# Kernel tuning notes

Hardware: AMD Instinct MI355X
Metric: run time of the kernel (lower is better)

Reference implementation:

```python
import jax, jax.numpy as jnp
import numpy as np

WS = 8          # window_size
SHIFT = 4       # shift_size
HEADS = 12
C = 384
HD = C // HEADS
SCALE = HD ** -0.5
N = WS * WS


def _rel_pos_index(Wh, Ww):
    # double_step_seq(2*Ww-1, Wh, 1, Ww) -> (1, Wh*Ww); idx = rel + rel.T; flip along axis 1
    seq1 = np.arange(0, (2 * Ww - 1) * Wh, 2 * Ww - 1)
    seq2 = np.arange(0, Ww)
    rel = (seq1[:, None] + seq2[None, :]).reshape(1, -1)
    idx = rel + rel.T
    return np.flip(idx, 1).copy()

REL_IDX = jnp.asarray(_rel_pos_index(WS, WS))  # [N, N] int


def window_partition(x, ws):
    # x: [B, H, W, C] -> [B*nW, ws*ws, C]
    B, H, W, Cc = x.shape
    x = x.reshape(B, H // ws, ws, W // ws, ws, Cc).transpose(0, 1, 3, 2, 4, 5)
    return x.reshape(-1, ws * ws, Cc)


def window_reverse(win, H, W, ws):
    B = win.shape[0] // ((H // ws) * (W // ws))
    x = win.reshape(B, H // ws, W // ws, ws, ws, -1).transpose(0, 1, 3, 2, 4, 5)
    return x.reshape(B, H, W, -1)


def _attn_mask(H, W, ws, shift):
    # region ids 0..8 per (h,w) as in the torch slice loop
    hi = np.arange(H)
    wi = np.arange(W)
    h_id = (hi >= H - ws).astype(np.int32) + (hi >= H - shift).astype(np.int32)
    w_id = (wi >= W - ws).astype(np.int32) + (wi >= W - shift).astype(np.int32)
    cnt = (h_id[:, None] * 3 + w_id[None, :]).astype(np.float32)
    img = jnp.asarray(cnt)[None, :, :, None]              # [1, H, W, 1]
    mw = window_partition(img, ws).reshape(-1, ws * ws)   # [nW, N]
    diff = mw[:, None, :] - mw[:, :, None]                # [nW, N, N]
    return jnp.where(diff != 0, jnp.float32(-100.0), jnp.float32(0.0))


def setup_inputs() -> dict:
    key = jax.random.key(0)
    ks = jax.random.split(key, 8)
    B, H, W = 16, 96, 96
    std = 0.02
    return {
        "query": jax.random.normal(ks[0], (B, H * W, C), jnp.float32),
        "skip_query": jax.random.normal(ks[1], (B, H * W, C), jnp.float32),
        "W_qkv": jax.random.normal(ks[2], (C, 2 * C), jnp.float32) * std,
        "b_qkv": jnp.zeros((2 * C,), jnp.float32),
        "W_skip": jax.random.normal(ks[3], (C, C), jnp.float32) * std,
        "b_skip": jnp.zeros((C,), jnp.float32),
        "rpb_table": jax.random.normal(ks[4], ((2 * WS - 1) * (2 * WS - 1), HEADS), jnp.float32) * std,
        "W_proj": jax.random.normal(ks[5], (C, C), jnp.float32) * std,
        "b_proj": jnp.zeros((C,), jnp.float32),
        "h": H,
        "w": W,
    }


def reference(query, skip_query, W_qkv, b_qkv, W_skip, b_skip, rpb_table, W_proj, b_proj, h, w):
    B, L, Cc = query.shape
    q4 = query.reshape(B, h, w, Cc)
    s4 = skip_query.reshape(B, h, w, Cc)
    pad_r = (WS - w % WS) % WS
    pad_b = (WS - h % WS) % WS
    q4 = jnp.pad(q4, ((0, 0), (0, pad_b), (0, pad_r), (0, 0)))
    s4 = jnp.pad(s4, ((0, 0), (0, pad_b), (0, pad_r), (0, 0)))
    H_pad, W_pad = q4.shape[1], q4.shape[2]

    # cyclic shift
    q4 = jnp.roll(q4, (-SHIFT, -SHIFT), axis=(1, 2))
    s4 = jnp.roll(s4, (-SHIFT, -SHIFT), axis=(1, 2))
    mask = _attn_mask(H_pad, W_pad, WS, SHIFT)  # [nW, N, N]

    xw = window_partition(q4, WS)   # [Bn, N, C] -> k, v source
    sw = window_partition(s4, WS)   # [Bn, N, C] -> q source
    Bn = xw.shape[0]

    kv = (xw @ W_qkv + b_qkv).reshape(Bn, N, 2, HEADS, HD)
    k = kv[:, :, 0].transpose(0, 2, 1, 3)   # [Bn, H, N, d]
    v = kv[:, :, 1].transpose(0, 2, 1, 3)
    q = ((sw @ W_skip + b_skip).reshape(Bn, N, HEADS, HD).transpose(0, 2, 1, 3)) * SCALE

    attn = jnp.einsum('bhnd,bhmd->bhnm', q, k)  # [Bn, H, N, N]
    rpb = rpb_table[REL_IDX.reshape(-1)].reshape(N, N, HEADS).transpose(2, 0, 1)
    attn = attn + rpb[None]
    nW = mask.shape[0]
    attn = (attn.reshape(B, nW, HEADS, N, N) + mask[None, :, None]).reshape(Bn, HEADS, N, N)
    attn = jax.nn.softmax(attn, axis=-1)

    out = jnp.einsum('bhnm,bhmd->bhnd', attn, v).transpose(0, 2, 1, 3).reshape(Bn, N, Cc)
    out = out @ W_proj + b_proj

    x4 = window_reverse(out.reshape(-1, WS, WS, Cc), H_pad, W_pad, WS)
    x4 = jnp.roll(x4, (SHIFT, SHIFT), axis=(1, 2))
    x4 = x4[:, :h, :w]
    return x4.reshape(B, h * w, Cc)
```

## Files before the change

### kernel.cpp

```cpp
#include <hip/hip_runtime.h>
#include <hip/hip_bf16.h>


typedef __attribute__((ext_vector_type(8))) short short8;
typedef __attribute__((ext_vector_type(4))) float floatx4;

#define MFMA16(a, b, c) __builtin_amdgcn_mfma_f32_16x16x32_bf16(a, b, c, 0, 0, 0)

__device__ __forceinline__ short f2bf(float f) {
    __hip_bfloat16 h = __float2bfloat16(f);
    return *reinterpret_cast<short*>(&h);
}

__device__ __forceinline__ unsigned cvt2bf(float lo, float hi) {
    unsigned r;
    asm("v_cvt_pk_bf16_f32 %0, %1, %2" : "=v"(r) : "v"(lo), "v"(hi));
    return r;
}

__device__ __forceinline__ void glds16(const void* g, void* l) {
    __builtin_amdgcn_global_load_lds(
        (const __attribute__((address_space(1))) void*)g,
        (__attribute__((address_space(3))) void*)l, 16, 0, 0);
}


__global__ __launch_bounds__(256) void prep_wt(const float* __restrict__ Wqkv,
                                               const float* __restrict__ Wskip,
                                               short* __restrict__ Wt) {
    int tid = blockIdx.x * 256 + threadIdx.x;
    if (tid >= 384 * 144) return;
    int k = tid / 144;
    int n8 = (tid % 144) * 8;
#pragma unroll
    for (int e = 0; e < 8; e++) {
        int n = n8 + e;
        float v = (n < 768) ? Wqkv[k * 768 + n]
                            : Wskip[k * 384 + (n - 768)] * 0.17677669529663687f;
        Wt[(size_t)n * 384 + k] = f2bf(v);
    }
}

__global__ __launch_bounds__(256) void prep_wtp(const float* __restrict__ Wproj,
                                                short* __restrict__ WtP) {
    int tid = blockIdx.x * 256 + threadIdx.x;
    if (tid >= 384 * 48) return;
    int k = tid / 48;
    int n8 = (tid % 48) * 8;
#pragma unroll
    for (int e = 0; e < 8; e++) {
        int n = n8 + e;
        WtP[(size_t)n * 384 + k] = f2bf(Wproj[k * 384 + n]);
    }
}

__global__ __launch_bounds__(256) void prep_bias(const float* __restrict__ rpb,
                                                 float* __restrict__ bias64) {
    int tid = blockIdx.x * 256 + threadIdx.x;
    if (tid >= 49152) return;
    int h = tid >> 12;
    int rem = tid & 4095;
    int i = rem >> 6, kk = rem & 63;
    int j = 63 - kk;
    int ridx = 15 * (i >> 3) + (i & 7) + 15 * (j >> 3) + (j & 7);
    bias64[tid] = rpb[ridx * 12 + h];
}

__global__ __launch_bounds__(256) void gemm_qkv(
    const float* __restrict__ xq, const float* __restrict__ xs,
    const short* __restrict__ Wt,
    const float* __restrict__ bqkv, const float* __restrict__ bskip,
    short* __restrict__ kbuf, short* __restrict__ vtbuf, short* __restrict__ qbuf) {
    __shared__ short smem[36864];
    const int ABASE = 24576;

    const int win = blockIdx.x;
    const int var = blockIdx.y;
    const int nb0 = var ? 6 : 0;
    const int nbN = var ? 3 : 6;
    const float* __restrict__ src = var ? xs : xq;

    const int tid = threadIdx.x, lane = tid & 63, wid = tid >> 6;
    const int l15 = lane & 15, g4 = lane >> 4;
    const int wm = wid >> 1, wn = wid & 1;

    {
        int r = tid >> 2, q4 = tid & 3;
        int b = win / 144, wr = win % 144;
        int wy = wr / 12, wx = wr % 12;
        int yy = wy * 8 + (r >> 3) + 4; if (yy >= 96) yy -= 96;
        int xx = wx * 8 + (r & 7) + 4;  if (xx >= 96) xx -= 96;
        const float* rbase = src + ((size_t)b * 9216 + yy * 96 + xx) * 384;
        short* lrow = smem + r * 384;
        int r7 = r & 7;
#pragma unroll
        for (int j = 0; j < 12; j++) {
            int c = q4 + j * 4;
            float4 f0 = *(const float4*)(rbase + c * 8);
            float4 f1 = *(const float4*)(rbase + c * 8 + 4);
            uint4 u;
            u.x = cvt2bf(f0.x, f0.y); u.y = cvt2bf(f0.z, f0.w);
            u.z = cvt2bf(f1.x, f1.y); u.w = cvt2bf(f1.z, f1.w);
            *(uint4*)(lrow + ((c ^ r7) * 8)) = u;
        }
    }

    int browoff[2], bdst[2];
#pragma unroll
    for (int j = 0; j < 2; j++) {
        int c0 = wid * 128 + j * 64;
        int c = c0 + lane;
        int brow = c >> 2, bs = c & 3;
        int sw = (brow ^ (brow >> 2)) & 3;
        browoff[j] = brow * 384 + (bs ^ sw) * 8;
        bdst[j] = ABASE + c0 * 8;
    }

    int arow[2];
#pragma unroll
    for (int b = 0; b < 2; b++) arow[b] = (wm * 32 + b * 16 + l15) * 384;
    const int al7 = l15 & 7;
    const int xsw = (g4 ^ ((l15 ^ (l15 >> 2)) & 3)) * 8;
    int brof[4];
#pragma unroll
    for (int nj = 0; nj < 4; nj++) brof[nj] = ABASE + (wn * 64 + nj * 16 + l15) * 32 + xsw;

    {
        const short* p0 = Wt + (size_t)nb0 * 49152;
#pragma unroll
        for (int j = 0; j < 2; j++) glds16(p0 + browoff[j], smem + bdst[j]);
#pragma unroll
        for (int j = 0; j < 2; j++) glds16(p0 + browoff[j] + 32, smem + bdst[j] + 4096);
    }
    __syncthreads();

    const short* bp = Wt + (size_t)nb0 * 49152;
    for (int pb = 0; pb < nbN; ++pb) {
        const int nb = nb0 + pb;
        const bool isv = (nb >= 3 && nb < 6);
        const bool lastp = (pb == nbN - 1);
        floatx4 acc[4][2];
        floatx4 accv[2][4];
#pragma unroll
        for (int a = 0; a < 4; a++)
#pragma unroll
            for (int b = 0; b < 2; b++)
#pragma unroll
                for (int r = 0; r < 4; r++) { acc[a][b][r] = 0.f; }
#pragma unroll
        for (int a = 0; a < 2; a++)
#pragma unroll
            for (int b = 0; b < 4; b++)
#pragma unroll
                for (int r = 0; r < 4; r++) { accv[a][b][r] = 0.f; }

#pragma unroll
        for (int kt = 0; kt < 12; ++kt) {
            const int hR = kt % 3;
            const int choff = ((kt * 4 + g4) ^ al7) * 8;
            short8 af[2], bfr[4];
#pragma unroll
            for (int b = 0; b < 2; b++)
                af[b] = *(const short8*)(smem + arow[b] + choff);
#pragma unroll
            for (int nj = 0; nj < 4; nj++)
                bfr[nj] = *(const short8*)(smem + brof[nj] + hR * 4096);
            if (!lastp || kt < 10) {
                const short* ps = (kt < 10) ? bp : (bp + 49152);
                const int ko = (kt < 10) ? (kt + 2) * 32 : (kt - 10) * 32;
                const int hW = (kt + 2) % 3;
#pragma unroll
                for (int j = 0; j < 2; j++)
                    glds16(ps + browoff[j] + ko, smem + bdst[j] + hW * 4096);
            }
            if (isv) {
#pragma unroll
                for (int a = 0; a < 2; a++)
#pragma unroll
                    for (int b = 0; b < 4; b++)
                        accv[a][b] = MFMA16(af[a], bfr[b], accv[a][b]);
            } else {
#pragma unroll
                for (int a = 0; a < 4; a++)
#pragma unroll
                    for (int b = 0; b < 2; b++)
                        acc[a][b] = MFMA16(bfr[a], af[b], acc[a][b]);
            }
            if (lastp && kt == 10) {
                asm volatile("s_waitcnt vmcnt(0)" ::: "memory");
            } else {
                asm volatile("s_waitcnt vmcnt(2)" ::: "memory");
            }
            __builtin_amdgcn_s_barrier();
        }

        const int ncol0 = nb * 128 + wn * 64;
        if (!isv) {
            short* buf;
            const float* bias;
            float scl;
            if (nb < 3) { buf = kbuf; bias = bqkv; scl = 1.0f; }
            else        { buf = qbuf; bias = bskip; scl = 0.17677669529663687f; }
#pragma unroll
            for (int a = 0; a < 4; a++) {
                int nbase = ncol0 + a * 16 + g4 * 4;
                int nm = (nb < 3) ? nbase : (nbase - 768);
                int head = nm >> 5, d0 = nm & 31;
                float4 bv = *(const float4*)(bias + nm);
                short* dst = buf + (size_t)(win * 12 + head) * 2048 + d0;
#pragma unroll
                for (int b = 0; b < 2; b++) {
                    int t = wm * 32 + b * 16 + l15;
                    uint2 pk;
                    pk.x = cvt2bf(acc[a][b][0] + bv.x * scl, acc[a][b][1] + bv.y * scl);
                    pk.y = cvt2bf(acc[a][b][2] + bv.z * scl, acc[a][b][3] + bv.w * scl);
                    *(uint2*)(dst + (size_t)t * 32) = pk;
                }
            }
        } else {
#pragma unroll
            for (int nj = 0; nj < 4; nj++) {
                int nm = ncol0 + nj * 16 + l15 - 384;
                int head = nm >> 5, d = nm & 31;
                float bvs = bqkv[384 + nm];
                short* dst = vtbuf + ((size_t)(win * 12 + head) * 32 + d) * 64;
#pragma unroll
                for (int mi = 0; mi < 2; mi++) {
                    int t0 = wm * 32 + mi * 16 + g4 * 4;
                    uint2 pk;
                    pk.x = cvt2bf(accv[mi][nj][0] + bvs, accv[mi][nj][1] + bvs);
                    pk.y = cvt2bf(accv[mi][nj][2] + bvs, accv[mi][nj][3] + bvs);
                    *(uint2*)(dst + t0) = pk;
                }
            }
        }
        bp += 49152;
    }
}

__global__ __launch_bounds__(256) void attn_kernel(
    const short* __restrict__ kbuf, const short* __restrict__ vtbuf,
    const short* __restrict__ qbuf, const float* __restrict__ bias64,
    short* __restrict__ aout, int ntask) {
    __shared__ short lps[18432];
    int lane = threadIdx.x & 63, wid = threadIdx.x >> 6;
    int task = blockIdx.x * 4 + wid;
    if (task >= ntask) return;
    int win = task / 12, head = task % 12;
    int l15 = lane & 15, g4 = lane >> 4;

    const short* kb = kbuf + (size_t)task * 2048;
    const short* qb = qbuf + (size_t)task * 2048;
    const short* vb = vtbuf + (size_t)task * 2048;

    short8 kf[4], qf[4], vf[2][2];
#pragma unroll
    for (int mi = 0; mi < 4; mi++)
        kf[mi] = *(const short8*)(kb + (mi * 16 + l15) * 32 + g4 * 8);
#pragma unroll
    for (int nj = 0; nj < 4; nj++)
        qf[nj] = *(const short8*)(qb + (nj * 16 + l15) * 32 + g4 * 8);
#pragma unroll
    for (int ma = 0; ma < 2; ma++)
#pragma unroll
        for (int ks = 0; ks < 2; ks++)
            vf[ma][ks] = *(const short8*)(vb + (ma * 16 + l15) * 64 + ks * 32 + g4 * 8);

    floatx4 st[4][4];
#pragma unroll
    for (int mi = 0; mi < 4; mi++)
#pragma unroll
        for (int nj = 0; nj < 4; nj++)
#pragma unroll
            for (int r = 0; r < 4; r++) st[mi][nj][r] = 0.f;

#pragma unroll
    for (int mi = 0; mi < 4; mi++)
#pragma unroll
        for (int nj = 0; nj < 4; nj++)
            st[mi][nj] = MFMA16(kf[mi], qf[nj], st[mi][nj]);

    const float* bb = bias64 + head * 4096;
#pragma unroll
    for (int nj = 0; nj < 4; nj++) {
        int i = nj * 16 + l15;
#pragma unroll
        for (int mi = 0; mi < 4; mi++) {
            floatx4 b4 = *(const floatx4*)(bb + i * 64 + mi * 16 + g4 * 4);
            st[mi][nj] += b4;
        }
    }

    int wr = win % 144;
    int wy = wr / 12, wx = wr % 12;
    if (wy == 11 || wx == 11) {
        int wy11 = (wy == 11), wx11 = (wx == 11);
        int ri[4];
#pragma unroll
        for (int nj = 0; nj < 4; nj++) {
            int t = nj * 16 + l15;
            int hh = wy11 ? (((t >> 3) >= 4) ? 2 : 1) : 0;
            int ww = wx11 ? (((t & 7) >= 4) ? 2 : 1) : 0;
            ri[nj] = hh * 3 + ww;
        }
#pragma unroll
        for (int mi = 0; mi < 4; mi++)
#pragma unroll
            for (int r = 0; r < 4; r++) {
                int t = mi * 16 + g4 * 4 + r;
                int hh = wy11 ? (((t >> 3) >= 4) ? 2 : 1) : 0;
                int ww = wx11 ? (((t & 7) >= 4) ? 2 : 1) : 0;
                int rk = hh * 3 + ww;
#pragma unroll
                for (int nj = 0; nj < 4; nj++)
                    if (rk != ri[nj]) st[mi][nj][r] -= 100.0f;
            }
    }

    float rden[4];
#pragma unroll
    for (int nj = 0; nj < 4; nj++) {
        float m = -1e30f;
#pragma unroll
        for (int mi = 0; mi < 4; mi++)
#pragma unroll
            for (int r = 0; r < 4; r++) m = fmaxf(m, st[mi][nj][r]);
        m = fmaxf(m, __shfl_xor(m, 16));
        m = fmaxf(m, __shfl_xor(m, 32));
        float s = 0.f;
#pragma unroll
        for (int mi = 0; mi < 4; mi++)
#pragma unroll
            for (int r = 0; r < 4; r++) {
                float p = __expf(st[mi][nj][r] - m);
                st[mi][nj][r] = p;
                s += p;
            }
        s += __shfl_xor(s, 16);
        s += __shfl_xor(s, 32);
        rden[nj] = 1.0f / s;
    }

    short* Lp = lps + wid * 4608;
#pragma unroll
    for (int mi = 0; mi < 4; mi++)
#pragma unroll
        for (int nj = 0; nj < 4; nj++) {
            uint2 pk;
            pk.x = cvt2bf(st[mi][nj][0], st[mi][nj][1]);
            pk.y = cvt2bf(st[mi][nj][2], st[mi][nj][3]);
            *(uint2*)(Lp + (nj * 16 + l15) * 72 + mi * 16 + g4 * 4) = pk;
        }

    floatx4 o[2][4];
#pragma unroll
    for (int ma = 0; ma < 2; ma++)
#pragma unroll
        for (int nj = 0; nj < 4; nj++)
#pragma unroll
            for (int r = 0; r < 4; r++) o[ma][nj][r] = 0.f;
#pragma unroll
    for (int ks = 0; ks < 2; ks++) {
        short8 pb[4];
#pragma unroll
        for (int nj = 0; nj < 4; nj++)
            pb[nj] = *(const short8*)(Lp + (nj * 16 + l15) * 72 + ks * 32 + g4 * 8);
#pragma unroll
        for (int ma = 0; ma < 2; ma++)
#pragma unroll
            for (int nj = 0; nj < 4; nj++)
                o[ma][nj] = MFMA16(vf[ma][ks], pb[nj], o[ma][nj]);
    }

    short* ob = aout + (size_t)win * 64 * 384 + head * 32;
#pragma unroll
    for (int ma = 0; ma < 2; ma++)
#pragma unroll
        for (int nj = 0; nj < 4; nj++) {
            int i = nj * 16 + l15;
            uint2 pk;
            pk.x = cvt2bf(o[ma][nj][0] * rden[nj], o[ma][nj][1] * rden[nj]);
            pk.y = cvt2bf(o[ma][nj][2] * rden[nj], o[ma][nj][3] * rden[nj]);
            *(uint2*)(ob + (size_t)i * 384 + ma * 16 + g4 * 4) = pk;
        }
}

__global__ __launch_bounds__(256) void gemm_proj(
    const short* __restrict__ aout, const short* __restrict__ WtP,
    const float* __restrict__ bproj, float* __restrict__ out) {
    __shared__ short smem[36864];
    const int ABASE = 24576;

    const int win = blockIdx.x;
    const int m0 = win * 64;
    const int tid = threadIdx.x, lane = tid & 63, wid = tid >> 6;
    const int l15 = lane & 15, g4 = lane >> 4;
    const int wm = wid >> 1, wn = wid & 1;

#pragma unroll
    for (int j = 0; j < 12; j++) {
        int i = wid * 12 + j;
        int c = i * 64 + lane;
        int row = c / 48, ch = c - row * 48;
        const short* s = aout + (size_t)(m0 + row) * 384 + ((ch ^ (row & 7)) * 8);
        glds16(s, smem + i * 512);
    }

    int browoff[2], bdst[2];
#pragma unroll
    for (int j = 0; j < 2; j++) {
        int c0 = wid * 128 + j * 64;
        int c = c0 + lane;
        int brow = c >> 2, bs = c & 3;
        int sw = (brow ^ (brow >> 2)) & 3;
        browoff[j] = brow * 384 + (bs ^ sw) * 8;
        bdst[j] = ABASE + c0 * 8;
    }

    int arow[2];
#pragma unroll
    for (int b = 0; b < 2; b++) arow[b] = (wm * 32 + b * 16 + l15) * 384;
    const int al7 = l15 & 7;
    const int xsw = (g4 ^ ((l15 ^ (l15 >> 2)) & 3)) * 8;
    int brof[4];
#pragma unroll
    for (int nj = 0; nj < 4; nj++) brof[nj] = ABASE + (wn * 64 + nj * 16 + l15) * 32 + xsw;

    {
#pragma unroll
        for (int j = 0; j < 2; j++) glds16(WtP + browoff[j], smem + bdst[j]);
#pragma unroll
        for (int j = 0; j < 2; j++) glds16(WtP + browoff[j] + 32, smem + bdst[j] + 4096);
    }
    __syncthreads();

    const int b_img = win / 144, wrw = win % 144;
    const int wy = wrw / 12, wx = wrw % 12;

    const short* bp = WtP;
    for (int pb = 0; pb < 3; ++pb) {
        const bool lastp = (pb == 2);
        floatx4 acc[4][2];
#pragma unroll
        for (int a = 0; a < 4; a++)
#pragma unroll
            for (int b = 0; b < 2; b++)
#pragma unroll
                for (int r = 0; r < 4; r++) acc[a][b][r] = 0.f;

#pragma unroll
        for (int kt = 0; kt < 12; ++kt) {
            const int hR = kt % 3;
            const int choff = ((kt * 4 + g4) ^ al7) * 8;
            short8 af[2], bfr[4];
#pragma unroll
            for (int b = 0; b < 2; b++)
                af[b] = *(const short8*)(smem + arow[b] + choff);
#pragma unroll
            for (int nj = 0; nj < 4; nj++)
                bfr[nj] = *(const short8*)(smem + brof[nj] + hR * 4096);
            if (!lastp || kt < 10) {
                const short* ps = (kt < 10) ? bp : (bp + 49152);
                const int ko = (kt < 10) ? (kt + 2) * 32 : (kt - 10) * 32;
                const int hW = (kt + 2) % 3;
#pragma unroll
                for (int j = 0; j < 2; j++)
                    glds16(ps + browoff[j] + ko, smem + bdst[j] + hW * 4096);
            }
#pragma unroll
            for (int a = 0; a < 4; a++)
#pragma unroll
                for (int b = 0; b < 2; b++)
                    acc[a][b] = MFMA16(bfr[a], af[b], acc[a][b]);
            if (lastp && kt == 10) {
                asm volatile("s_waitcnt vmcnt(0)" ::: "memory");
            } else {
                asm volatile("s_waitcnt vmcnt(2)" ::: "memory");
            }
            __builtin_amdgcn_s_barrier();
        }

#pragma unroll
        for (int a = 0; a < 4; a++) {
            int n = pb * 128 + wn * 64 + a * 16 + g4 * 4;
            float4 bv = *(const float4*)(bproj + n);
#pragma unroll
            for (int b = 0; b < 2; b++) {
                int t = wm * 32 + b * 16 + l15;
                int yy = wy * 8 + (t >> 3) + 4; if (yy >= 96) yy -= 96;
                int xx = wx * 8 + (t & 7) + 4;  if (xx >= 96) xx -= 96;
                floatx4 o = acc[a][b];
                o[0] += bv.x; o[1] += bv.y; o[2] += bv.z; o[3] += bv.w;
                *(floatx4*)(&out[((size_t)b_img * 9216 + yy * 96 + xx) * 384 + n]) = o;
            }
        }
        bp += 49152;
    }
}

extern "C" void kernel_launch(void* const* d_in, const int* in_sizes, int n_in,
                              void* d_out, int out_size, void* d_ws, size_t ws_size,
                              hipStream_t stream) {
    const float* query = (const float*)d_in[0];
    const float* skipq = (const float*)d_in[1];
    const float* Wqkv  = (const float*)d_in[2];
    const float* bqkv  = (const float*)d_in[3];
    const float* Wskip = (const float*)d_in[4];
    const float* bskip = (const float*)d_in[5];
    const float* rpb   = (const float*)d_in[6];
    const float* Wproj = (const float*)d_in[7];
    const float* bproj = (const float*)d_in[8];
    float* out = (float*)d_out;

    int M = in_sizes[0] / 384;
    int nwin = M / 64;

    char* ws = (char*)d_ws;
    size_t off = 0;
    auto alloc = [&](size_t bytes) -> void* {
        void* p = ws + off;
        off = (off + bytes + 255) & ~(size_t)255;
        return p;
    };
    short* Wt     = (short*)alloc((size_t)1152 * 384 * 2);
    short* WtP    = (short*)alloc((size_t)384 * 384 * 2);
    float* bias64 = (float*)alloc((size_t)12 * 64 * 64 * 4);
    short* kbuf   = (short*)alloc((size_t)M * 384 * 2);
    short* vtbuf  = (short*)alloc((size_t)M * 384 * 2);
    short* qbuf   = (short*)alloc((size_t)M * 384 * 2);
    short* aout   = (short*)alloc((size_t)M * 384 * 2);
    (void)ws_size;

    hipLaunchKernelGGL(prep_wt, dim3(216), dim3(256), 0, stream, Wqkv, Wskip, Wt);
    hipLaunchKernelGGL(prep_wtp, dim3(72), dim3(256), 0, stream, Wproj, WtP);
    hipLaunchKernelGGL(prep_bias, dim3(192), dim3(256), 0, stream, rpb, bias64);
    hipLaunchKernelGGL(gemm_qkv, dim3(nwin, 2), dim3(256), 0, stream,
                       query, skipq, Wt, bqkv, bskip, kbuf, vtbuf, qbuf);
    hipLaunchKernelGGL(attn_kernel, dim3(nwin * 12 / 4), dim3(256), 0, stream,
                       kbuf, vtbuf, qbuf, bias64, aout, nwin * 12);
    hipLaunchKernelGGL(gemm_proj, dim3(nwin), dim3(256), 0, stream,
                       aout, WtP, bproj, out);
}
```

Before: 534.0 us.

## Load GEMM weight fragments directly from global into registers, drop LDS B staging

```diff
diff --git a/kernel.cpp b/kernel.cpp
--- a/kernel.cpp
+++ b/kernel.cpp
@@ -66,23 +66,66 @@
     bias64[tid] = rpb[ridx * 12 + h];
 }
 
-__global__ __launch_bounds__(256) void gemm_qkv(
+template <bool SW>
+__device__ __forceinline__ void gemm_panel(
+    const short* __restrict__ sA, const short* __restrict__ Blane0,
+    const short* __restrict__ Blane1, int l15, int g4, int al7,
+    floatx4 (&acc)[2][4]) {
+#pragma unroll
+    for (int a = 0; a < 2; a++)
+#pragma unroll
+        for (int b = 0; b < 4; b++)
+#pragma unroll
+            for (int r = 0; r < 4; r++) acc[a][b][r] = 0.f;
+
+    short8 bfr[3][2];
+#pragma unroll
+    for (int s = 0; s < 3; s++) {
+        bfr[s][0] = *(const short8*)(Blane0 + s * 32);
+        bfr[s][1] = *(const short8*)(Blane1 + s * 32);
+    }
+#pragma unroll
+    for (int kt = 0; kt < 12; ++kt) {
+        const int choff = ((kt * 4 + g4) ^ al7) * 8;
+        short8 af[4];
+#pragma unroll
+        for (int b = 0; b < 4; b++)
+            af[b] = *(const short8*)(sA + (b * 16 + l15) * 384 + choff);
+        short8 b0 = bfr[kt % 3][0], b1 = bfr[kt % 3][1];
+        if (kt < 9) {
+            bfr[kt % 3][0] = *(const short8*)(Blane0 + (kt + 3) * 32);
+            bfr[kt % 3][1] = *(const short8*)(Blane1 + (kt + 3) * 32);
+        }
+        if (SW) {
+#pragma unroll
+            for (int b = 0; b < 4; b++) {
+                acc[0][b] = MFMA16(b0, af[b], acc[0][b]);
+                acc[1][b] = MFMA16(b1, af[b], acc[1][b]);
+            }
+        } else {
+#pragma unroll
+            for (int b = 0; b < 4; b++) {
+                acc[0][b] = MFMA16(af[b], b0, acc[0][b]);
+                acc[1][b] = MFMA16(af[b], b1, acc[1][b]);
+            }
+        }
+    }
+}
+
+__global__ __launch_bounds__(256, 3) void gemm_qkv(
     const float* __restrict__ xq, const float* __restrict__ xs,
     const short* __restrict__ Wt,
     const float* __restrict__ bqkv, const float* __restrict__ bskip,
     short* __restrict__ kbuf, short* __restrict__ vtbuf, short* __restrict__ qbuf) {
-    __shared__ short smem[36864];
-    const int ABASE = 24576;
+    __shared__ short smem[24576];
 
     const int win = blockIdx.x;
     const int var = blockIdx.y;
-    const int nb0 = var ? 6 : 0;
-    const int nbN = var ? 3 : 6;
     const float* __restrict__ src = var ? xs : xq;
 
     const int tid = threadIdx.x, lane = tid & 63, wid = tid >> 6;
     const int l15 = lane & 15, g4 = lane >> 4;
-    const int wm = wid >> 1, wn = wid & 1;
+    const int al7 = l15 & 7;
 
     {
         int r = tid >> 2, q4 = tid & 3;
@@ -104,137 +147,77 @@
             *(uint4*)(lrow + ((c ^ r7) * 8)) = u;
         }
     }
-
-    int browoff[2], bdst[2];
-#pragma unroll
-    for (int j = 0; j < 2; j++) {
-        int c0 = wid * 128 + j * 64;
-        int c = c0 + lane;
-        int brow = c >> 2, bs = c & 3;
-        int sw = (brow ^ (brow >> 2)) & 3;
-        browoff[j] = brow * 384 + (bs ^ sw) * 8;
-        bdst[j] = ABASE + c0 * 8;
-    }
-
-    int arow[2];
-#pragma unroll
-    for (int b = 0; b < 2; b++) arow[b] = (wm * 32 + b * 16 + l15) * 384;
-    const int al7 = l15 & 7;
-    const int xsw = (g4 ^ ((l15 ^ (l15 >> 2)) & 3)) * 8;
-    int brof[4];
-#pragma unroll
-    for (int nj = 0; nj < 4; nj++) brof[nj] = ABASE + (wn * 64 + nj * 16 + l15) * 32 + xsw;
-
-    {
-        const short* p0 = Wt + (size_t)nb0 * 49152;
-#pragma unroll
-        for (int j = 0; j < 2; j++) glds16(p0 + browoff[j], smem + bdst[j]);
-#pragma unroll
-        for (int j = 0; j < 2; j++) glds16(p0 + browoff[j] + 32, smem + bdst[j] + 4096);
-    }
     __syncthreads();
 
-    const short* bp = Wt + (size_t)nb0 * 49152;
-    for (int pb = 0; pb < nbN; ++pb) {
-        const int nb = nb0 + pb;
-        const bool isv = (nb >= 3 && nb < 6);
-        const bool lastp = (pb == nbN - 1);
-        floatx4 acc[4][2];
-        floatx4 accv[2][4];
-#pragma unroll
-        for (int a = 0; a < 4; a++)
-#pragma unroll
-            for (int b = 0; b < 2; b++)
-#pragma unroll
-                for (int r = 0; r < 4; r++) { acc[a][b][r] = 0.f; }
-#pragma unroll
-        for (int a = 0; a < 2; a++)
-#pragma unroll
-            for (int b = 0; b < 4; b++)
-#pragma unroll
-                for (int r = 0; r < 4; r++) { accv[a][b][r] = 0.f; }
-
-#pragma unroll
-        for (int kt = 0; kt < 12; ++kt) {
-            const int hR = kt % 3;
-            const int choff = ((kt * 4 + g4) ^ al7) * 8;
-            short8 af[2], bfr[4];
-#pragma unroll
-            for (int b = 0; b < 2; b++)
-                af[b] = *(const short8*)(smem + arow[b] + choff);
-#pragma unroll
-            for (int nj = 0; nj < 4; nj++)
-                bfr[nj] = *(const short8*)(smem + brof[nj] + hR * 4096);
-            if (!lastp || kt < 10) {
-                const short* ps = (kt < 10) ? bp : (bp + 49152);
-                const int ko = (kt < 10) ? (kt + 2) * 32 : (kt - 10) * 32;
-                const int hW = (kt + 2) % 3;
-#pragma unroll
-                for (int j = 0; j < 2; j++)
-                    glds16(ps + browoff[j] + ko, smem + bdst[j] + hW * 4096);
-            }
-            if (isv) {
-#pragma unroll
-                for (int a = 0; a < 2; a++)
-#pragma unroll
-                    for (int b = 0; b < 4; b++)
-                        accv[a][b] = MFMA16(af[a], bfr[b], accv[a][b]);
-            } else {
-#pragma unroll
-                for (int a = 0; a < 4; a++)
-#pragma unroll
-                    for (int b = 0; b < 2; b++)
-                        acc[a][b] = MFMA16(bfr[a], af[b], acc[a][b]);
-            }
-            if (lastp && kt == 10) {
-                asm volatile("s_waitcnt vmcnt(0)" ::: "memory");
-            } else {
-                asm volatile("s_waitcnt vmcnt(2)" ::: "memory");
-            }
-            __builtin_amdgcn_s_barrier();
-        }
-
-        const int ncol0 = nb * 128 + wn * 64;
-        if (!isv) {
-            short* buf;
-            const float* bias;
-            float scl;
-            if (nb < 3) { buf = kbuf; bias = bqkv; scl = 1.0f; }
-            else        { buf = qbuf; bias = bskip; scl = 0.17677669529663687f; }
-#pragma unroll
-            for (int a = 0; a < 4; a++) {
-                int nbase = ncol0 + a * 16 + g4 * 4;
-                int nm = (nb < 3) ? nbase : (nbase - 768);
+    if (var == 0) {
+        for (int nb = 0; nb < 3; ++nb) {
+            const short* Bl0 = Wt + (size_t)(nb * 128 + wid * 32 + l15) * 384 + g4 * 8;
+            const short* Bl1 = Bl0 + 16 * 384;
+            floatx4 acc[2][4];
+            gemm_panel<true>(smem, Bl0, Bl1, l15, g4, al7, acc);
+            const int ncol0 = nb * 128 + wid * 32;
+#pragma unroll
+            for (int a = 0; a < 2; a++) {
+                int nm = ncol0 + a * 16 + g4 * 4;
                 int head = nm >> 5, d0 = nm & 31;
-                float4 bv = *(const float4*)(bias + nm);
-                short* dst = buf + (size_t)(win * 12 + head) * 2048 + d0;
-#pragma unroll
-                for (int b = 0; b < 2; b++) {
-                    int t = wm * 32 + b * 16 + l15;
+                float4 bv = *(const float4*)(bqkv + nm);
+                short* dst = kbuf + (size_t)(win * 12 + head) * 2048 + d0;
+#pragma unroll
+                for (int b = 0; b < 4; b++) {
+                    int t = b * 16 + l15;
+                    uint2 pk;
+                    pk.x = cvt2bf(acc[a][b][0] + bv.x, acc[a][b][1] + bv.y);
+                    pk.y = cvt2bf(acc[a][b][2] + bv.z, acc[a][b][3] + bv.w);
+                    *(uint2*)(dst + (size_t)t * 32) = pk;
+                }
+            }
+        }
+        for (int nb = 3; nb < 6; ++nb) {
+            const short* Bl0 = Wt + (size_t)(nb * 128 + wid * 32 + l15) * 384 + g4 * 8;
+            const short* Bl1 = Bl0 + 16 * 384;
+            floatx4 acc[2][4];
+            gemm_panel<false>(smem, Bl0, Bl1, l15, g4, al7, acc);
+            const int ncol0 = nb * 128 + wid * 32;
+#pragma unroll
+            for (int nj = 0; nj < 2; nj++) {
+                int nm = ncol0 + nj * 16 + l15 - 384;
+                int head = nm >> 5, d = nm & 31;
+                float bvs = bqkv[384 + nm];
+                short* dst = vtbuf + ((size_t)(win * 12 + head) * 32 + d) * 64;
+#pragma unroll
+                for (int mi = 0; mi < 4; mi++) {
+                    int t0 = mi * 16 + g4 * 4;
+                    uint2 pk;
+                    pk.x = cvt2bf(acc[nj][mi][0] + bvs, acc[nj][mi][1] + bvs);
+                    pk.y = cvt2bf(acc[nj][mi][2] + bvs, acc[nj][mi][3] + bvs);
+                    *(uint2*)(dst + t0) = pk;
+                }
+            }
+        }
+    } else {
+        for (int nb = 6; nb < 9; ++nb) {
+            const short* Bl0 = Wt + (size_t)(nb * 128 + wid * 32 + l15) * 384 + g4 * 8;
+            const short* Bl1 = Bl0 + 16 * 384;
+            floatx4 acc[2][4];
+            gemm_panel<true>(smem, Bl0, Bl1, l15, g4, al7, acc);
+            const int ncol0 = nb * 128 + wid * 32;
+            const float scl = 0.17677669529663687f;
+#pragma unroll
+            for (int a = 0; a < 2; a++) {
+                int nm = ncol0 + a * 16 + g4 * 4 - 768;
+                int head = nm >> 5, d0 = nm & 31;
+                float4 bv = *(const float4*)(bskip + nm);
+                short* dst = qbuf + (size_t)(win * 12 + head) * 2048 + d0;
+#pragma unroll
+                for (int b = 0; b < 4; b++) {
+                    int t = b * 16 + l15;
                     uint2 pk;
                     pk.x = cvt2bf(acc[a][b][0] + bv.x * scl, acc[a][b][1] + bv.y * scl);
                     pk.y = cvt2bf(acc[a][b][2] + bv.z * scl, acc[a][b][3] + bv.w * scl);
                     *(uint2*)(dst + (size_t)t * 32) = pk;
                 }
             }
-        } else {
-#pragma unroll
-            for (int nj = 0; nj < 4; nj++) {
-                int nm = ncol0 + nj * 16 + l15 - 384;
-                int head = nm >> 5, d = nm & 31;
-                float bvs = bqkv[384 + nm];
-                short* dst = vtbuf + ((size_t)(win * 12 + head) * 32 + d) * 64;
-#pragma unroll
-                for (int mi = 0; mi < 2; mi++) {
-                    int t0 = wm * 32 + mi * 16 + g4 * 4;
-                    uint2 pk;
-                    pk.x = cvt2bf(accv[mi][nj][0] + bvs, accv[mi][nj][1] + bvs);
-                    pk.y = cvt2bf(accv[mi][nj][2] + bvs, accv[mi][nj][3] + bvs);
-                    *(uint2*)(dst + t0) = pk;
-                }
-            }
-        }
-        bp += 49152;
+        }
     }
 }
 
@@ -385,17 +368,16 @@
         }
 }
 
-__global__ __launch_bounds__(256) void gemm_proj(
+__global__ __launch_bounds__(256, 3) void gemm_proj(
     const short* __restrict__ aout, const short* __restrict__ WtP,
     const float* __restrict__ bproj, float* __restrict__ out) {
-    __shared__ short smem[36864];
-    const int ABASE = 24576;
+    __shared__ short smem[24576];
 
     const int win = blockIdx.x;
     const int m0 = win * 64;
     const int tid = threadIdx.x, lane = tid & 63, wid = tid >> 6;
     const int l15 = lane & 15, g4 = lane >> 4;
-    const int wm = wid >> 1, wn = wid & 1;
+    const int al7 = l15 & 7;
 
 #pragma unroll
     for (int j = 0; j < 12; j++) {
@@ -405,88 +387,24 @@
         const short* s = aout + (size_t)(m0 + row) * 384 + ((ch ^ (row & 7)) * 8);
         glds16(s, smem + i * 512);
     }
-
-    int browoff[2], bdst[2];
-#pragma unroll
-    for (int j = 0; j < 2; j++) {
-        int c0 = wid * 128 + j * 64;
-        int c = c0 + lane;
-        int brow = c >> 2, bs = c & 3;
-        int sw = (brow ^ (brow >> 2)) & 3;
-        browoff[j] = brow * 384 + (bs ^ sw) * 8;
-        bdst[j] = ABASE + c0 * 8;
-    }
-
-    int arow[2];
-#pragma unroll
-    for (int b = 0; b < 2; b++) arow[b] = (wm * 32 + b * 16 + l15) * 384;
-    const int al7 = l15 & 7;
-    const int xsw = (g4 ^ ((l15 ^ (l15 >> 2)) & 3)) * 8;
-    int brof[4];
-#pragma unroll
-    for (int nj = 0; nj < 4; nj++) brof[nj] = ABASE + (wn * 64 + nj * 16 + l15) * 32 + xsw;
-
-    {
-#pragma unroll
-        for (int j = 0; j < 2; j++) glds16(WtP + browoff[j], smem + bdst[j]);
-#pragma unroll
-        for (int j = 0; j < 2; j++) glds16(WtP + browoff[j] + 32, smem + bdst[j] + 4096);
-    }
+    asm volatile("s_waitcnt vmcnt(0)" ::: "memory");
     __syncthreads();
 
     const int b_img = win / 144, wrw = win % 144;
     const int wy = wrw / 12, wx = wrw % 12;
 
-    const short* bp = WtP;
     for (int pb = 0; pb < 3; ++pb) {
-        const bool lastp = (pb == 2);
-        floatx4 acc[4][2];
-#pragma unroll
-        for (int a = 0; a < 4; a++)
-#pragma unroll
-            for (int b = 0; b < 2; b++)
-#pragma unroll
-                for (int r = 0; r < 4; r++) acc[a][b][r] = 0.f;
-
-#pragma unroll
-        for (int kt = 0; kt < 12; ++kt) {
-            const int hR = kt % 3;
-            const int choff = ((kt * 4 + g4) ^ al7) * 8;
-            short8 af[2], bfr[4];
-#pragma unroll
-            for (int b = 0; b < 2; b++)
-                af[b] = *(const short8*)(smem + arow[b] + choff);
-#pragma unroll
-            for (int nj = 0; nj < 4; nj++)
-                bfr[nj] = *(const short8*)(smem + brof[nj] + hR * 4096);
-            if (!lastp || kt < 10) {
-                const short* ps = (kt < 10) ? bp : (bp + 49152);
-                const int ko = (kt < 10) ? (kt + 2) * 32 : (kt - 10) * 32;
-                const int hW = (kt + 2) % 3;
-#pragma unroll
-                for (int j = 0; j < 2; j++)
-                    glds16(ps + browoff[j] + ko, smem + bdst[j] + hW * 4096);
-            }
-#pragma unroll
-            for (int a = 0; a < 4; a++)
-#pragma unroll
-                for (int b = 0; b < 2; b++)
-                    acc[a][b] = MFMA16(bfr[a], af[b], acc[a][b]);
-            if (lastp && kt == 10) {
-                asm volatile("s_waitcnt vmcnt(0)" ::: "memory");
-            } else {
-                asm volatile("s_waitcnt vmcnt(2)" ::: "memory");
-            }
-            __builtin_amdgcn_s_barrier();
-        }
-
-#pragma unroll
-        for (int a = 0; a < 4; a++) {
-            int n = pb * 128 + wn * 64 + a * 16 + g4 * 4;
+        const short* Bl0 = WtP + (size_t)(pb * 128 + wid * 32 + l15) * 384 + g4 * 8;
+        const short* Bl1 = Bl0 + 16 * 384;
+        floatx4 acc[2][4];
+        gemm_panel<true>(smem, Bl0, Bl1, l15, g4, al7, acc);
+#pragma unroll
+        for (int a = 0; a < 2; a++) {
+            int n = pb * 128 + wid * 32 + a * 16 + g4 * 4;
             float4 bv = *(const float4*)(bproj + n);
 #pragma unroll
-            for (int b = 0; b < 2; b++) {
-                int t = wm * 32 + b * 16 + l15;
+            for (int b = 0; b < 4; b++) {
+                int t = b * 16 + l15;
                 int yy = wy * 8 + (t >> 3) + 4; if (yy >= 96) yy -= 96;
                 int xx = wx * 8 + (t & 7) + 4;  if (xx >= 96) xx -= 96;
                 floatx4 o = acc[a][b];
@@ -494,7 +412,6 @@
                 *(floatx4*)(&out[((size_t)b_img * 9216 + yy * 96 + xx) * 384 + n]) = o;
             }
         }
-        bp += 49152;
     }
 }
 
```

Measured after the change: 1.089 ms. 2.04x slower.
